# Optimization experiments

Hardware: AMD Instinct MI355X
Metric: run time of the kernel (lower is better)

## Reference

```python
import jax, jax.numpy as jnp
import numpy as np

VOCAB, EMB, H, TRK, L, BOUND = 50257, 1024, 1024, 1024, 256, 25

def setup_inputs() -> dict:
    key = jax.random.key(0)
    ks = jax.random.split(key, 16)
    s = 0.02
    return {
        "query_words": jax.random.normal(ks[0], (L, 1, H), jnp.float32),
        "query_vector": jax.random.normal(ks[1], (1, 1, TRK), jnp.float32),
        "decision_vector": jax.random.normal(ks[2], (1, 1, H), jnp.float32),
        "target_answer": jax.random.randint(ks[3], (BOUND, 1, 1), 0, VOCAB, jnp.int64),
        "emb_table": jax.random.normal(ks[4], (VOCAB, EMB), jnp.float32) * s,
        "gru_Wih": jax.random.normal(ks[5], (3 * H, EMB + TRK), jnp.float32) * s,
        "gru_Whh": jax.random.normal(ks[6], (3 * H, H), jnp.float32) * s,
        "gru_bih": jnp.zeros((3 * H,), jnp.float32),
        "gru_bhh": jnp.zeros((3 * H,), jnp.float32),
        "attn_Wq": jax.random.normal(ks[7], (H, H), jnp.float32) * s,
        "attn_bq": jnp.zeros((H,), jnp.float32),
        "attn_Wk": jax.random.normal(ks[8], (H, H), jnp.float32) * s,
        "attn_bk": jnp.zeros((H,), jnp.float32),
        "attn_v": jax.random.normal(ks[9], (H,), jnp.float32) * s,
        "concat_W": jax.random.normal(ks[10], (H, 2 * H), jnp.float32) * s,
        "concat_b": jnp.zeros((H,), jnp.float32),
        "out_W": jax.random.normal(ks[11], (VOCAB, H), jnp.float32) * s,
        "out_b": jnp.zeros((VOCAB,), jnp.float32),
    }


def reference(query_words, query_vector, decision_vector, target_answer,
              emb_table, gru_Wih, gru_Whh, gru_bih, gru_bhh,
              attn_Wq, attn_bq, attn_Wk, attn_bk, attn_v,
              concat_W, concat_b, out_W, out_b):
    # eval-mode: dropout = identity; tf_ratio=1 -> teacher forcing for all steps
    h_dim = decision_vector.shape[-1]
    qw = query_words[:, 0, :]                      # [L, H] encoder memory
    keys = qw @ attn_Wk.T + attn_bk                # precompute key projection once
    qv = query_vector.reshape(-1)                  # [TRK]
    h0 = decision_vector.reshape(-1)               # [H]
    ta = target_answer.reshape(-1).astype(jnp.int32)
    # input token per step: SOS (0), then teacher-forced targets
    idx_seq = jnp.concatenate([jnp.zeros((1,), jnp.int32), ta[: BOUND - 1]])

    def step(h, idx):
        x = jnp.concatenate([qv, emb_table[idx]])  # cat(query_vector, embedded)
        g = gru_Wih @ x + gru_bih                  # [3H]
        gh = gru_Whh @ h + gru_bhh                 # [3H]
        r = jax.nn.sigmoid(g[:h_dim] + gh[:h_dim])
        z = jax.nn.sigmoid(g[h_dim:2 * h_dim] + gh[h_dim:2 * h_dim])
        n = jnp.tanh(g[2 * h_dim:] + r * gh[2 * h_dim:])
        h_new = (1.0 - z) * n + z * h
        # additive (Bahdanau) attention over query_words
        e = jnp.tanh(keys + attn_Wq @ h_new + attn_bq) @ attn_v  # [L]
        w = jax.nn.softmax(e)
        ctx = w @ qw                                              # [H]
        vec = jnp.tanh(concat_W @ jnp.concatenate([h_new, ctx]) + concat_b)
        logits = out_W @ vec + out_b                              # [VOCAB]
        return h_new, jax.nn.log_softmax(logits)

    _, logps = jax.lax.scan(step, h0, idx_seq)     # [BOUND, VOCAB]
    answer = jnp.argmax(logps, axis=-1)            # greedy tokens per step
    return (answer, logps)
```

## Files before the change

### kernel.cpp

```cpp
#include <hip/hip_runtime.h>
#include <math.h>

#define VOCAB 50257
#define EMB 1024
#define HD 1024
#define TRK 1024
#define LQ 256
#define BND 25
#define SENT 0xAAAAAAAAu

__device__ __forceinline__ float wred(float s){
  #pragma unroll
  for (int m = 32; m >= 1; m >>= 1) s += __shfl_xor(s, m, 64);
  return s;
}

__global__ __launch_bounds__(256) void k_pre_keys(const float* __restrict__ Wih,
                                                  const float* __restrict__ qv,
                                                  const float* __restrict__ bih,
                                                  const int*   __restrict__ ta,
                                                  const float* __restrict__ emb,
                                                  const float* __restrict__ qw,
                                                  const float* __restrict__ Wk,
                                                  float* __restrict__ gib,
                                                  float* __restrict__ E,
                                                  float* __restrict__ part){
  __shared__ float qt[64*256];
  int b = blockIdx.x, tid = threadIdx.x;
  if (b < 768){
    int w = tid >> 6, lane = tid & 63;
    int row = b*4 + w;
    const float* a = Wih + (size_t)row*2048;
    float s = 0.f;
    #pragma unroll
    for (int e = 0; e < 4; e++){
      int k = e*256 + lane*4;
      float4 av = *(const float4*)(a + k);
      float4 qr = *(const float4*)(qv + k);
      s += av.x*qr.x + av.y*qr.y + av.z*qr.z + av.w*qr.w;
    }
    s = wred(s);
    if (lane == 0) gib[row] = s + bih[row];
    return;
  }
  if (b < 868){
    int g = (b - 768)*256 + tid;
    int t = g >> 10, i = g & 1023;
    int idx = (t == 0) ? 0 : ta[t-1];
    E[g] = emb[(size_t)idx*EMB + i];
    return;
  }
  int b2 = b - 868;
  int jb = b2 & 63;
  int ks = b2 >> 6;
  int l = tid;
  float acc[16];
  #pragma unroll
  for (int j = 0; j < 16; j++) acc[j] = 0.f;

  for (int kt = 0; kt < 4; kt++){
    int kb = ks*256 + kt*64;
    __syncthreads();
    #pragma unroll
    for (int p = 0; p < 16; p++){
      int fidx = (p*256 + tid)*4;
      int kk = fidx & 63, ll = fidx >> 6;
      float4 v = *(const float4*)(qw + (size_t)ll*1024 + kb + kk);
      qt[(kk+0)*256 + (ll ^ ((kk+0)&31))] = v.x;
      qt[(kk+1)*256 + (ll ^ ((kk+1)&31))] = v.y;
      qt[(kk+2)*256 + (ll ^ ((kk+2)&31))] = v.z;
      qt[(kk+3)*256 + (ll ^ ((kk+3)&31))] = v.w;
    }
    __syncthreads();
    #pragma unroll
    for (int s = 0; s < 4; s++){
      float qr[16];
      #pragma unroll
      for (int q = 0; q < 16; q++){
        int k = s*16 + q;
        qr[q] = qt[k*256 + (l ^ (k&31))];
      }
      #pragma unroll
      for (int j = 0; j < 16; j++){
        const float* wr = Wk + (size_t)(jb*16 + j)*1024 + kb + s*16;
        #pragma unroll
        for (int q4 = 0; q4 < 4; q4++){
          float4 wv = *(const float4*)(wr + q4*4);
          acc[j] += qr[q4*4+0]*wv.x + qr[q4*4+1]*wv.y
                  + qr[q4*4+2]*wv.z + qr[q4*4+3]*wv.w;
        }
      }
    }
  }
  #pragma unroll
  for (int j = 0; j < 16; j++)
    part[((size_t)ks*1024 + jb*16 + j)*256 + l] = acc[j];
}

template<int K, int NCH>
__global__ __launch_bounds__(256) void k_gemm_s2(const float* __restrict__ A, int lda,
                                                 const float* __restrict__ B, int ldb,
                                                 const float* __restrict__ bias,
                                                 float* __restrict__ C,
                                                 int R, int N, int act){
  __shared__ float Bl[NCH*K];
  constexpr int KD4 = K/4;
  int tid = threadIdx.x, w = tid >> 6, lane = tid & 63;
  int row = blockIdx.x*4 + w;
  const float* a = A + (size_t)row*lda;
  float4 ar[K/256];
  #pragma unroll
  for (int e = 0; e < K/256; e++)
    ar[e] = *(const float4*)(a + e*256 + lane*4);
  float bs = bias[row];
  for (int c0 = 0; c0 < N; c0 += NCH){
    int nt = min(NCH, N - c0);
    __syncthreads();
    int total = nt*KD4;
    for (int i = tid; i < total; i += 256){
      int j = i/KD4, kk = i - j*KD4;
      *(float4*)&Bl[j*K + kk*4] = *(const float4*)(B + (size_t)(c0+j)*ldb + kk*4);
    }
    __syncthreads();
    for (int j = 0; j < nt; j++){
      float s = 0.f;
      #pragma unroll
      for (int e = 0; e < K/256; e++){
        float4 bv = *(const float4*)&Bl[j*K + e*256 + lane*4];
        s += ar[e].x*bv.x + ar[e].y*bv.y + ar[e].z*bv.z + ar[e].w*bv.w;
      }
      s = wred(s);
      if (lane == 0){
        float v = s + bs;
        if (act) v = tanhf(v);
        C[(size_t)(c0+j)*R + row] = v;
      }
    }
  }
}

__global__ __launch_bounds__(512, 1) void k_gru6(const float* __restrict__ Whh,
                                                 const float* __restrict__ bhh,
                                                 const float* __restrict__ gi,
                                                 const float* __restrict__ dv,
                                                 float* __restrict__ HC,
                                                 unsigned* __restrict__ hxu){
  __shared__ float Wl[24][1024];
  __shared__ float hbuf[1024];
  __shared__ float sres[24];
  int tid = threadIdx.x, w = tid >> 6, lane = tid & 63;
  int b = blockIdx.x;
  for (int i = tid; i < 6144; i += 512){
    int r = i >> 8, c = (i & 255)*4;
    int g = r >> 3, s = r & 7;
    *(float4*)&Wl[r][c] = *(const float4*)(Whh + (size_t)(g*1024 + b*8 + s)*1024 + c);
  }
  if (tid < 256)
    *(float4*)&hbuf[tid*4] = *(const float4*)(dv + tid*4);
  __syncthreads();

  for (int t = 0; t < BND; t++){
    float g0=0,g1=0,g2=0,bb0=0,bb1=0,bb2=0,hpown=0;
    if (tid < 8){
      int i = b*8 + tid;
      const float* gg = gi + (size_t)t*3072;
      g0 = gg[i]; g1 = gg[1024+i]; g2 = gg[2048+i];
      bb0 = bhh[i]; bb1 = bhh[1024+i]; bb2 = bhh[2048+i];
      hpown = hbuf[i];
    }
    float hv[16];
    #pragma unroll
    for (int e = 0; e < 4; e++){
      float4 v = *(const float4*)&hbuf[e*256 + lane*4];
      hv[e*4]=v.x; hv[e*4+1]=v.y; hv[e*4+2]=v.z; hv[e*4+3]=v.w;
    }
    #pragma unroll
    for (int j = 0; j < 3; j++){
      int r = w*3 + j;
      float a = 0.f;
      #pragma unroll
      for (int e = 0; e < 4; e++){
        float4 v = *(const float4*)&Wl[r][e*256 + lane*4];
        a += v.x*hv[e*4] + v.y*hv[e*4+1] + v.z*hv[e*4+2] + v.w*hv[e*4+3];
      }
      a = wred(a);
      if (lane == 0) sres[r] = a;
    }
    __syncthreads();
    if (tid < 8){
      int i = b*8 + tid;
      float ghr = sres[tid]      + bb0;
      float ghz = sres[8  + tid] + bb1;
      float ghn = sres[16 + tid] + bb2;
      float rr = 1.f/(1.f + expf(-(g0 + ghr)));
      float zz = 1.f/(1.f + expf(-(g1 + ghz)));
      float nn = tanhf(g2 + rr*ghn);
      float hnew = (1.f - zz)*nn + zz*hpown;
      HC[(size_t)t*2048 + i] = hnew;
      if (t < BND-1){
        union { float f; unsigned u; } cv; cv.f = hnew;
        if (cv.u == SENT) cv.u ^= 1u;
        __hip_atomic_store(hxu + (size_t)t*2048 + b*16 + tid, cv.u,
                           __ATOMIC_RELAXED, __HIP_MEMORY_SCOPE_AGENT);
        asm volatile("s_waitcnt vmcnt(0)" ::: "memory");
      }
    }
    if (t == BND-1) break;
    if (w == 0){
      const unsigned* base = hxu + (size_t)t*2048;
      #pragma unroll
      for (int q = 0; q < 2; q++){
        int blk = q*64 + lane;
        const unsigned* bp = base + blk*16;
        unsigned d[8];
        for (;;){
          bool ok = true;
          #pragma unroll
          for (int j = 0; j < 8; j++){
            d[j] = __hip_atomic_load(bp + j, __ATOMIC_RELAXED, __HIP_MEMORY_SCOPE_AGENT);
            ok = ok && (d[j] != SENT);
          }
          if (ok) break;
        }
        #pragma unroll
        for (int j = 0; j < 8; j++)
          hbuf[blk*8 + j] = __uint_as_float(d[j]);
      }
    }
    __syncthreads();
  }
}

__global__ __launch_bounds__(256) void k_attn1(const float* __restrict__ part,
                                               const float* __restrict__ bk,
                                               const float* __restrict__ Qt,
                                               const float* __restrict__ av,
                                               float* __restrict__ epart){
  int t = blockIdx.x, jc = blockIdx.y;
  int l = threadIdx.x;
  const float* q = Qt + (size_t)t*1024;
  int j0 = jc*32;
  float acc = 0.f;
  #pragma unroll
  for (int u = 0; u < 8; u++){
    #pragma unroll
    for (int v = 0; v < 4; v++){
      int j = j0 + u*4 + v;
      float kv = part[(size_t)j*256 + l]
               + part[(size_t)(1024+j)*256 + l]
               + part[(size_t)(2048+j)*256 + l]
               + part[(size_t)(3072+j)*256 + l]
               + bk[j];
      acc += tanhf(kv + q[j]) * av[j];
    }
  }
  epart[((size_t)t*32 + jc)*256 + l] = acc;
}

__global__ __launch_bounds__(256) void k_attn2(const float* __restrict__ epart,
                                               const float* __restrict__ qw,
                                               float* __restrict__ HC){
  __shared__ float red[256];
  __shared__ float sw[256];
  int t = blockIdx.x, tid = threadIdx.x;
  float e = 0.f;
  for (int jc = 0; jc < 32; jc++) e += epart[((size_t)t*32 + jc)*256 + tid];
  red[tid] = e; __syncthreads();
  for (int s = 128; s > 0; s >>= 1){
    if (tid < s) red[tid] = fmaxf(red[tid], red[tid+s]);
    __syncthreads();
  }
  float m = red[0]; __syncthreads();
  float wv = expf(e - m);
  red[tid] = wv; __syncthreads();
  for (int s = 128; s > 0; s >>= 1){
    if (tid < s) red[tid] += red[tid+s];
    __syncthreads();
  }
  float inv = 1.f/red[0];
  sw[tid] = wv*inv; __syncthreads();
  float4 c = make_float4(0.f,0.f,0.f,0.f);
  const float* qp = qw + tid*4;
  for (int ll = 0; ll < 256; ll++){
    float wl = sw[ll];
    float4 v = *(const float4*)(qp + (size_t)ll*1024);
    c.x += wl*v.x; c.y += wl*v.y; c.z += wl*v.z; c.w += wl*v.w;
  }
  *(float4*)(HC + (size_t)t*2048 + 1024 + tid*4) = c;
}

__global__ __launch_bounds__(256, 1) void k_gemm_big9(const float* __restrict__ A,
                                                      const float* __restrict__ B,
                                                      const float* __restrict__ bias,
                                                      float* __restrict__ C){
  __shared__ float Bl[25600];
  int tid = threadIdx.x;
  int rl = tid & 63;
  int q  = tid >> 6;
  int R0 = blockIdx.x*256;

  for (int i = tid; i < 6400; i += 256){
    int t = i >> 8, kk = (i & 255) << 2;
    *(float4*)&Bl[t*1024 + kk] = *(const float4*)(B + (size_t)t*1024 + kk);
  }

  const float* ap[4];
  #pragma unroll
  for (int j = 0; j < 4; j++){
    int r = R0 + 64*j + rl;
    if (r >= VOCAB) r = VOCAB-1;
    ap[j] = A + (size_t)r*1024 + q*256;
  }

  float acc[4][25];
  #pragma unroll
  for (int j = 0; j < 4; j++)
    #pragma unroll
    for (int t = 0; t < 25; t++) acc[j][t] = 0.f;

  float4 a[4][4];
  #pragma unroll
  for (int j = 0; j < 4; j++){
    a[j][0] = *(const float4*)(ap[j] + 0);
    a[j][1] = *(const float4*)(ap[j] + 4);
    a[j][2] = *(const float4*)(ap[j] + 8);
    a[j][3] = *(const float4*)(ap[j] + 12);
  }
  __syncthreads();

  const float* bq = Bl + q*256;
  #pragma unroll 1
  for (int kb = 0; kb < 256; kb += 16){
    float4 n[4][4];
    if (kb + 16 < 256){
      #pragma unroll
      for (int j = 0; j < 4; j++){
        n[j][0] = *(const float4*)(ap[j] + kb + 16);
        n[j][1] = *(const float4*)(ap[j] + kb + 20);
        n[j][2] = *(const float4*)(ap[j] + kb + 24);
        n[j][3] = *(const float4*)(ap[j] + kb + 28);
      }
    }
    #pragma unroll
    for (int t = 0; t < 25; t++){
      const float* bt = bq + t*1024 + kb;
      float4 b0 = *(const float4*)(bt + 0);
      float4 b1 = *(const float4*)(bt + 4);
      float4 b2 = *(const float4*)(bt + 8);
      float4 b3 = *(const float4*)(bt + 12);
      #pragma unroll
      for (int j = 0; j < 4; j++){
        acc[j][t] += a[j][0].x*b0.x + a[j][0].y*b0.y + a[j][0].z*b0.z + a[j][0].w*b0.w
                   + a[j][1].x*b1.x + a[j][1].y*b1.y + a[j][1].z*b1.z + a[j][1].w*b1.w
                   + a[j][2].x*b2.x + a[j][2].y*b2.y + a[j][2].z*b2.z + a[j][2].w*b2.w
                   + a[j][3].x*b3.x + a[j][3].y*b3.y + a[j][3].z*b3.z + a[j][3].w*b3.w;
      }
    }
    #pragma unroll
    for (int j = 0; j < 4; j++){
      a[j][0] = n[j][0]; a[j][1] = n[j][1]; a[j][2] = n[j][2]; a[j][3] = n[j][3];
    }
  }

  for (int tc0 = 0; tc0 < 25; tc0 += 13){
    int nt = min(13, 25 - tc0);
    __syncthreads();
    #pragma unroll
    for (int j = 0; j < 4; j++)
      for (int tt = 0; tt < nt; tt++)
        Bl[(q*256 + j*64 + rl)*13 + tt] = acc[j][tc0 + tt];
    __syncthreads();
    for (int v = tid; v < 256*nt; v += 256){
      int rr = v & 255, tt = v >> 8;
      float s = 0.f;
      #pragma unroll
      for (int qq = 0; qq < 4; qq++)
        s += Bl[(qq*256 + rr)*13 + tt];
      int row = R0 + rr;
      if (row < VOCAB)
        C[(size_t)(tc0 + tt)*VOCAB + row] = s + bias[row];
    }
  }
}

__global__ __launch_bounds__(256) void k_lstat(const float* __restrict__ C,
                                               float* __restrict__ pm,
                                               float* __restrict__ ps,
                                               int*   __restrict__ pa){
  __shared__ float sm[256], ss[256];
  __shared__ int   sa[256];
  int t = blockIdx.x, c = blockIdx.y, tid = threadIdx.x;
  int r0 = c*6283, r1 = min(r0 + 6283, VOCAB);
  const float* p = C + (size_t)t*VOCAB;
  float m = -3.4e38f, s = 0.f; int arg = r0;
  for (int r = r0 + tid; r < r1; r += 256){
    float x = p[r];
    if (x > m){ s = s*expf(m - x) + 1.f; m = x; arg = r; }
    else       s += expf(x - m);
  }
  sm[tid] = m; ss[tid] = s; sa[tid] = arg; __syncthreads();
  for (int st = 128; st > 0; st >>= 1){
    if (tid < st){
      float m1 = sm[tid], s1 = ss[tid]; int a1 = sa[tid];
      float m2 = sm[tid+st], s2 = ss[tid+st]; int a2 = sa[tid+st];
      if (m2 > m1){ sm[tid] = m2; ss[tid] = s2 + s1*expf(m1 - m2); sa[tid] = a2; }
      else if (m2 == m1){ ss[tid] = s1 + s2; sa[tid] = min(a1, a2); }
      else { ss[tid] = s1 + s2*expf(m2 - m1); }
    }
    __syncthreads();
  }
  if (tid == 0){ pm[t*8 + c] = sm[0]; ps[t*8 + c] = ss[0]; pa[t*8 + c] = sa[0]; }
}

__global__ __launch_bounds__(256) void k_lsub2(float* __restrict__ C,
                                               const float* __restrict__ pm,
                                               const float* __restrict__ ps,
                                               const int* __restrict__ pa,
                                               float* __restrict__ out){
  int t = blockIdx.y;
  float M = pm[t*8], S = ps[t*8]; int A = pa[t*8];
  #pragma unroll
  for (int c = 1; c < 8; c++){
    float m2 = pm[t*8+c], s2 = ps[t*8+c]; int a2 = pa[t*8+c];
    if (m2 > M){ S = s2 + S*expf(M - m2); M = m2; A = a2; }
    else if (m2 == M){ S += s2; A = min(A, a2); }
    else S += s2*expf(m2 - M);
  }
  float Lg = logf(S) + M;
  int r = blockIdx.x*256 + threadIdx.x;
  if (r < VOCAB) C[(size_t)t*VOCAB + r] -= Lg;
  if (blockIdx.x == 0 && threadIdx.x == 0) out[t] = (float)A;
}

extern "C" void kernel_launch(void* const* d_in, const int* in_sizes, int n_in,
                              void* d_out, int out_size, void* d_ws, size_t ws_size,
                              hipStream_t stream){
  const float* qw  = (const float*)d_in[0];
  const float* qv  = (const float*)d_in[1];
  const float* dv  = (const float*)d_in[2];
  const int*   ta  = (const int*)d_in[3];
  const float* emb = (const float*)d_in[4];
  const float* Wih = (const float*)d_in[5];
  const float* Whh = (const float*)d_in[6];
  const float* bih = (const float*)d_in[7];
  const float* bhh = (const float*)d_in[8];
  const float* Wq  = (const float*)d_in[9];
  const float* bq  = (const float*)d_in[10];
  const float* Wk  = (const float*)d_in[11];
  const float* bk  = (const float*)d_in[12];
  const float* av  = (const float*)d_in[13];
  const float* cW  = (const float*)d_in[14];
  const float* cb  = (const float*)d_in[15];
  const float* oW  = (const float*)d_in[16];
  const float* ob  = (const float*)d_in[17];
  float* out = (float*)d_out;
  float* ws  = (float*)d_ws;

  float* part  = ws;
  float* ep    = ws + 1048576;
  float* E     = ws + 1310720;
  float* gib   = ws + 1336320;
  float* gi    = ws + 1339392;
  float* HC    = ws + 1416192;
  float* Qt    = ws + 1467392;
  float* VEC   = ws + 1492992;
  unsigned* hx = (unsigned*)(ws + 1518592);
  float* pm    = ws + 1569792;
  float* ps    = ws + 1570048;
  int*   pa    = (int*)(ws + 1570304);

  hipMemsetAsync(hx, 0xAA, 51200*4, stream);
  k_pre_keys<<<1124, 256, 0, stream>>>(Wih, qv, bih, ta, emb, qw, Wk, gib, E, part);
  k_gemm_s2<1024,16><<<768, 256, 0, stream>>>(Wih + 1024, 2048, E, 1024, gib, gi, 3072, 25, 0);
  k_gru6<<<128, 512, 0, stream>>>(Whh, bhh, gi, dv, HC, hx);
  k_gemm_s2<1024,16><<<256, 256, 0, stream>>>(Wq, 1024, HC, 2048, bq, Qt, 1024, 25, 0);
  k_attn1<<<dim3(25,32), 256, 0, stream>>>(part, bk, Qt, av, ep);
  k_attn2<<<25, 256, 0, stream>>>(ep, qw, HC);
  k_gemm_s2<2048,8><<<256, 256, 0, stream>>>(cW, 2048, HC, 2048, cb, VEC, 1024, 25, 1);
  k_gemm_big9<<<197, 256, 0, stream>>>(oW, VEC, ob, out + 25);
  k_lstat<<<dim3(25,8), 256, 0, stream>>>(out + 25, pm, ps, pa);
  k_lsub2<<<dim3(197,25), 256, 0, stream>>>(out + 25, pm, ps, pa, out);
}
```

Baseline: 415.1 us.

## Double waves per block in vocab GEMM and batch GRU sync polling

The output-projection GEMM now runs 512 threads per block, each handling 2 rows instead of 4, which halves per-thread accumulator registers and removes the software prefetch of A. The reduction layout is adjusted to match. In the GRU kernel, the wait after each hidden-state store is dropped, and the two polling loops over peer blocks are merged so all 16 loads go out together. This trades register-level prefetching for more resident waves, and it relies on relaxed atomics staying visible without the explicit store wait.

```diff
diff --git a/kernel.cpp b/kernel.cpp
--- a/kernel.cpp
+++ b/kernel.cpp
@@ -139,7 +139,7 @@
   }
 }
 
-__global__ __launch_bounds__(512, 1) void k_gru6(const float* __restrict__ Whh,
+__global__ __launch_bounds__(512, 1) void k_gru7(const float* __restrict__ Whh,
                                                  const float* __restrict__ bhh,
                                                  const float* __restrict__ gi,
                                                  const float* __restrict__ dv,
@@ -202,29 +202,29 @@
         if (cv.u == SENT) cv.u ^= 1u;
         __hip_atomic_store(hxu + (size_t)t*2048 + b*16 + tid, cv.u,
                            __ATOMIC_RELAXED, __HIP_MEMORY_SCOPE_AGENT);
-        asm volatile("s_waitcnt vmcnt(0)" ::: "memory");
       }
     }
     if (t == BND-1) break;
     if (w == 0){
       const unsigned* base = hxu + (size_t)t*2048;
-      #pragma unroll
-      for (int q = 0; q < 2; q++){
-        int blk = q*64 + lane;
-        const unsigned* bp = base + blk*16;
-        unsigned d[8];
-        for (;;){
-          bool ok = true;
-          #pragma unroll
-          for (int j = 0; j < 8; j++){
-            d[j] = __hip_atomic_load(bp + j, __ATOMIC_RELAXED, __HIP_MEMORY_SCOPE_AGENT);
-            ok = ok && (d[j] != SENT);
-          }
-          if (ok) break;
+      const unsigned* bp0 = base + lane*16;
+      const unsigned* bp1 = base + (64 + lane)*16;
+      unsigned d[16];
+      for (;;){
+        bool ok = true;
+        #pragma unroll
+        for (int j = 0; j < 8; j++){
+          d[j]   = __hip_atomic_load(bp0 + j, __ATOMIC_RELAXED, __HIP_MEMORY_SCOPE_AGENT);
+          d[8+j] = __hip_atomic_load(bp1 + j, __ATOMIC_RELAXED, __HIP_MEMORY_SCOPE_AGENT);
         }
         #pragma unroll
-        for (int j = 0; j < 8; j++)
-          hbuf[blk*8 + j] = __uint_as_float(d[j]);
+        for (int j = 0; j < 16; j++) ok = ok && (d[j] != SENT);
+        if (ok) break;
+      }
+      #pragma unroll
+      for (int j = 0; j < 8; j++){
+        hbuf[lane*8 + j]        = __uint_as_float(d[j]);
+        hbuf[(64+lane)*8 + j]   = __uint_as_float(d[8+j]);
       }
     }
     __syncthreads();
@@ -289,57 +289,48 @@
   *(float4*)(HC + (size_t)t*2048 + 1024 + tid*4) = c;
 }
 
-__global__ __launch_bounds__(256, 1) void k_gemm_big9(const float* __restrict__ A,
-                                                      const float* __restrict__ B,
-                                                      const float* __restrict__ bias,
-                                                      float* __restrict__ C){
-  __shared__ float Bl[25600];
+__global__ __launch_bounds__(512, 1) void k_gemm_big14(const float* __restrict__ A,
+                                                       const float* __restrict__ B,
+                                                       const float* __restrict__ bias,
+                                                       float* __restrict__ C){
+  __shared__ float Bl[26624];
   int tid = threadIdx.x;
   int rl = tid & 63;
-  int q  = tid >> 6;
+  int w  = tid >> 6;
+  int p  = w >> 1;
+  int sub = w & 1;
   int R0 = blockIdx.x*256;
 
-  for (int i = tid; i < 6400; i += 256){
+  for (int i = tid; i < 6400; i += 512){
     int t = i >> 8, kk = (i & 255) << 2;
     *(float4*)&Bl[t*1024 + kk] = *(const float4*)(B + (size_t)t*1024 + kk);
   }
 
-  const float* ap[4];
-  #pragma unroll
-  for (int j = 0; j < 4; j++){
-    int r = R0 + 64*j + rl;
+  const float* ap[2];
+  #pragma unroll
+  for (int j = 0; j < 2; j++){
+    int r = R0 + sub*128 + j*64 + rl;
     if (r >= VOCAB) r = VOCAB-1;
-    ap[j] = A + (size_t)r*1024 + q*256;
-  }
-
-  float acc[4][25];
-  #pragma unroll
-  for (int j = 0; j < 4; j++)
+    ap[j] = A + (size_t)r*1024 + p*256;
+  }
+
+  float acc[2][25];
+  #pragma unroll
+  for (int j = 0; j < 2; j++)
     #pragma unroll
     for (int t = 0; t < 25; t++) acc[j][t] = 0.f;
-
-  float4 a[4][4];
-  #pragma unroll
-  for (int j = 0; j < 4; j++){
-    a[j][0] = *(const float4*)(ap[j] + 0);
-    a[j][1] = *(const float4*)(ap[j] + 4);
-    a[j][2] = *(const float4*)(ap[j] + 8);
-    a[j][3] = *(const float4*)(ap[j] + 12);
-  }
   __syncthreads();
 
-  const float* bq = Bl + q*256;
+  const float* bq = Bl + p*256;
   #pragma unroll 1
   for (int kb = 0; kb < 256; kb += 16){
-    float4 n[4][4];
-    if (kb + 16 < 256){
-      #pragma unroll
-      for (int j = 0; j < 4; j++){
-        n[j][0] = *(const float4*)(ap[j] + kb + 16);
-        n[j][1] = *(const float4*)(ap[j] + kb + 20);
-        n[j][2] = *(const float4*)(ap[j] + kb + 24);
-        n[j][3] = *(const float4*)(ap[j] + kb + 28);
-      }
+    float4 a[2][4];
+    #pragma unroll
+    for (int j = 0; j < 2; j++){
+      a[j][0] = *(const float4*)(ap[j] + kb + 0);
+      a[j][1] = *(const float4*)(ap[j] + kb + 4);
+      a[j][2] = *(const float4*)(ap[j] + kb + 8);
+      a[j][3] = *(const float4*)(ap[j] + kb + 12);
     }
     #pragma unroll
     for (int t = 0; t < 25; t++){
@@ -349,33 +340,30 @@
       float4 b2 = *(const float4*)(bt + 8);
       float4 b3 = *(const float4*)(bt + 12);
       #pragma unroll
-      for (int j = 0; j < 4; j++){
+      for (int j = 0; j < 2; j++){
         acc[j][t] += a[j][0].x*b0.x + a[j][0].y*b0.y + a[j][0].z*b0.z + a[j][0].w*b0.w
                    + a[j][1].x*b1.x + a[j][1].y*b1.y + a[j][1].z*b1.z + a[j][1].w*b1.w
                    + a[j][2].x*b2.x + a[j][2].y*b2.y + a[j][2].z*b2.z + a[j][2].w*b2.w
                    + a[j][3].x*b3.x + a[j][3].y*b3.y + a[j][3].z*b3.z + a[j][3].w*b3.w;
       }
     }
-    #pragma unroll
-    for (int j = 0; j < 4; j++){
-      a[j][0] = n[j][0]; a[j][1] = n[j][1]; a[j][2] = n[j][2]; a[j][3] = n[j][3];
-    }
   }
 
   for (int tc0 = 0; tc0 < 25; tc0 += 13){
     int nt = min(13, 25 - tc0);
     __syncthreads();
     #pragma unroll
-    for (int j = 0; j < 4; j++)
+    for (int j = 0; j < 2; j++)
       for (int tt = 0; tt < nt; tt++)
-        Bl[(q*256 + j*64 + rl)*13 + tt] = acc[j][tc0 + tt];
-    __syncthreads();
-    for (int v = tid; v < 256*nt; v += 256){
+        Bl[(w*128 + j*64 + rl)*13 + tt] = acc[j][tc0 + tt];
+    __syncthreads();
+    for (int v = tid; v < 256*nt; v += 512){
       int rr = v & 255, tt = v >> 8;
+      int sb = rr >> 7, lr = rr & 127;
       float s = 0.f;
       #pragma unroll
-      for (int qq = 0; qq < 4; qq++)
-        s += Bl[(qq*256 + rr)*13 + tt];
+      for (int pp = 0; pp < 4; pp++)
+        s += Bl[((pp*2 + sb)*128 + lr)*13 + tt];
       int row = R0 + rr;
       if (row < VOCAB)
         C[(size_t)(tc0 + tt)*VOCAB + row] = s + bias[row];
@@ -472,12 +460,12 @@
   hipMemsetAsync(hx, 0xAA, 51200*4, stream);
   k_pre_keys<<<1124, 256, 0, stream>>>(Wih, qv, bih, ta, emb, qw, Wk, gib, E, part);
   k_gemm_s2<1024,16><<<768, 256, 0, stream>>>(Wih + 1024, 2048, E, 1024, gib, gi, 3072, 25, 0);
-  k_gru6<<<128, 512, 0, stream>>>(Whh, bhh, gi, dv, HC, hx);
+  k_gru7<<<128, 512, 0, stream>>>(Whh, bhh, gi, dv, HC, hx);
   k_gemm_s2<1024,16><<<256, 256, 0, stream>>>(Wq, 1024, HC, 2048, bq, Qt, 1024, 25, 0);
   k_attn1<<<dim3(25,32), 256, 0, stream>>>(part, bk, Qt, av, ep);
   k_attn2<<<25, 256, 0, stream>>>(ep, qw, HC);
   k_gemm_s2<2048,8><<<256, 256, 0, stream>>>(cW, 2048, HC, 2048, cb, VEC, 1024, 25, 1);
-  k_gemm_big9<<<197, 256, 0, stream>>>(oW, VEC, ob, out + 25);
+  k_gemm_big14<<<197, 512, 0, stream>>>(oW, VEC, ob, out + 25);
   k_lstat<<<dim3(25,8), 256, 0, stream>>>(out + 25, pm, ps, pa);
   k_lsub2<<<dim3(197,25), 256, 0, stream>>>(out + 25, pm, ps, pa, out);
 }
```

Result: slower. 548.7 us (+32.2%).
